# Optimization experiments

Hardware: AMD Instinct MI355X
Metric: run time of the kernel (lower is better)

## Reference

```python
import jax, jax.numpy as jnp
import numpy as np

N, E, IDIM, HLD, H, ODIM = 40000, 640000, 64, 128, 2, 1


def setup_inputs() -> dict:
    key = jax.random.key(0)
    ks = jax.random.split(key, 16)
    g = lambda i, shape, scale=0.05: (jax.random.normal(ks[i], shape, jnp.float32) * scale)
    return {
        "x": jax.random.normal(ks[0], (N, IDIM), jnp.float32),
        "edgeIdx": jax.random.randint(ks[1], (2, E), 0, N, dtype=jnp.int32),
        "edgeAttr": jax.random.normal(ks[2], (E, 4), jnp.float32),  # unused by model (passed as None)
        "enc_w0": g(3, (IDIM, HLD)), "enc_b0": jnp.zeros((HLD,), jnp.float32),
        "enc_w1": g(4, (HLD, HLD)), "enc_b1": jnp.zeros((HLD,), jnp.float32),
        "gat0_W": g(5, (HLD, H * HLD)), "gat0_bl": jnp.zeros((H * HLD,), jnp.float32),
        "gat0_att": g(6, (H, HLD)), "gat0_bias": jnp.zeros((HLD,), jnp.float32),
        "gat1_W": g(7, (HLD, H * HLD)), "gat1_bl": jnp.zeros((H * HLD,), jnp.float32),
        "gat1_att": g(8, (H, HLD)), "gat1_bias": jnp.zeros((HLD,), jnp.float32),
        "dec_w0": g(9, (HLD, HLD)), "dec_b0": jnp.zeros((HLD,), jnp.float32),
        "dec_w1": g(10, (HLD, ODIM)), "dec_b1": jnp.zeros((ODIM,), jnp.float32),
    }


def _gatv2(x, src, dst, W, bl, att, bias):
    # GATv2Conv, share_weights=True, concat=False, add_self_loops=False
    h = (x @ W + bl).reshape(N, H, HLD)                      # [N,H,C]
    e = jax.nn.leaky_relu(h[src] + h[dst], negative_slope=0.2)  # [E,H,C]
    scores = jnp.einsum('ehc,hc->eh', e, att)                # [E,H]
    m = jax.ops.segment_max(scores, dst, num_segments=N)     # per-target max
    ex = jnp.exp(scores - m[dst])
    den = jax.ops.segment_sum(ex, dst, num_segments=N)
    alpha = ex / (den[dst] + 1e-16)                          # edge softmax [E,H]
    out = jax.ops.segment_sum(alpha[:, :, None] * h[src], dst, num_segments=N)
    return out.mean(axis=1) + bias, alpha


def reference(x, edgeIdx, edgeAttr, enc_w0, enc_b0, enc_w1, enc_b1,
              gat0_W, gat0_bl, gat0_att, gat0_bias,
              gat1_W, gat1_bl, gat1_att, gat1_bias,
              dec_w0, dec_b0, dec_w1, dec_b1):
    src, dst = edgeIdx[0], edgeIdx[1]
    h = jax.nn.silu(x @ enc_w0 + enc_b0)
    h = jax.nn.silu(h @ enc_w1 + enc_b1)
    h, alpha = _gatv2(h, src, dst, gat0_W, gat0_bl, gat0_att, gat0_bias)
    h = jax.nn.silu(h)
    h, alpha = _gatv2(h, src, dst, gat1_W, gat1_bl, gat1_att, gat1_bias)
    h = jax.nn.silu(h)
    h = h @ dec_w0 + dec_b0   # decode MLP has no activations
    h = h @ dec_w1 + dec_b1
    return h, alpha.mean(axis=1)
```

## Files before the change

### kernel.cpp

```cpp
#include <hip/hip_runtime.h>
#include <hip/hip_bf16.h>
#include <math.h>

#define NN 40000
#define EE 640000
#define IDIM 64
#define HLD 128
#define NH 2
#define HH 256

typedef __attribute__((ext_vector_type(8))) short short8;
typedef __attribute__((ext_vector_type(4))) float f32x4;

__device__ __forceinline__ float silu_f(float v) {
    return v / (1.0f + expf(-v));
}
__device__ __forceinline__ unsigned short f2bf(float f) {
    unsigned u = __float_as_uint(f);
    unsigned r = (u + 0x7FFFu + ((u >> 16) & 1u)) >> 16;
    return (unsigned short)r;
}
__device__ __forceinline__ float bf2f(unsigned short b) {
    return __uint_as_float((unsigned)b << 16);
}

__global__ void k_count(const int* __restrict__ dst, int* __restrict__ counts) {
    int e = blockIdx.x * 256 + threadIdx.x;
    if (e < EE) atomicAdd(&counts[dst[e]], 1);
}

__global__ void k_blocksum(const int* __restrict__ counts, int* __restrict__ bsum) {
    __shared__ int s[256];
    int t = threadIdx.x;
    int i = blockIdx.x * 256 + t;
    s[t] = (i < NN) ? counts[i] : 0;
    __syncthreads();
    for (int o = 128; o > 0; o >>= 1) {
        if (t < o) s[t] += s[t + o];
        __syncthreads();
    }
    if (t == 0) bsum[blockIdx.x] = s[0];
}

__global__ void k_scanb(int* __restrict__ bsum, int nb) {
    __shared__ int s[256];
    int t = threadIdx.x;
    int v = (t < nb) ? bsum[t] : 0;
    s[t] = v;
    __syncthreads();
    for (int o = 1; o < 256; o <<= 1) {
        int x = 0;
        if (t >= o) x = s[t - o];
        __syncthreads();
        s[t] += x;
        __syncthreads();
    }
    if (t < nb) bsum[t] = s[t] - v;
}

__global__ void k_scatter(const int* __restrict__ counts, const int* __restrict__ bsum,
                          int* __restrict__ offsets) {
    __shared__ int s[256];
    int t = threadIdx.x;
    int i = blockIdx.x * 256 + t;
    int v = (i < NN) ? counts[i] : 0;
    s[t] = v;
    __syncthreads();
    for (int o = 1; o < 256; o <<= 1) {
        int x = 0;
        if (t >= o) x = s[t - o];
        __syncthreads();
        s[t] += x;
        __syncthreads();
    }
    if (i < NN) offsets[i] = s[t] - v + bsum[blockIdx.x];
    if (i == 0) offsets[NN] = EE;
}

__global__ void k_fill(const int* __restrict__ dst, const int* __restrict__ src,
                       const int* __restrict__ offsets,
                       int* __restrict__ cursor, int* __restrict__ ebd,
                       int* __restrict__ ebs) {
    int e = blockIdx.x * 256 + threadIdx.x;
    if (e >= EE) return;
    int d = dst[e];
    int pos = offsets[d] + atomicAdd(&cursor[d], 1);
    ebd[pos] = e;
    ebs[pos] = src[e];
}

__global__ void k_cvtX(const float* __restrict__ in, unsigned short* __restrict__ out, int n4) {
    int i = blockIdx.x * 256 + threadIdx.x;
    if (i >= n4) return;
    float4 v = *(const float4*)(in + (size_t)i * 4);
    ushort4 o;
    o.x = f2bf(v.x); o.y = f2bf(v.y); o.z = f2bf(v.z); o.w = f2bf(v.w);
    *(ushort4*)(out + (size_t)i * 4) = o;
}

__global__ void k_cvtB(const float* __restrict__ W, unsigned short* __restrict__ out,
                       int K, int N) {
    int KB = K / 32;
    int total = (N / 16) * KB * 64;
    int idx = blockIdx.x * 256 + threadIdx.x;
    if (idx >= total) return;
    int lane = idx & 63;
    int t = idx >> 6;
    int kb = t % KB, nb = t / KB;
    int n = nb * 16 + (lane & 15);
    int kbase = kb * 32 + (lane >> 4) * 8;
    unsigned short tmp[8];
    #pragma unroll
    for (int j = 0; j < 8; j++) tmp[j] = f2bf(W[(size_t)(kbase + j) * N + n]);
    uint4 o;
    o.x = (unsigned)tmp[0] | ((unsigned)tmp[1] << 16);
    o.y = (unsigned)tmp[2] | ((unsigned)tmp[3] << 16);
    o.z = (unsigned)tmp[4] | ((unsigned)tmp[5] << 16);
    o.w = (unsigned)tmp[6] | ((unsigned)tmp[7] << 16);
    *(uint4*)(out + (size_t)idx * 8) = o;
}

template <int ACT, int KB, int NB>
__global__ __launch_bounds__(256) void k_mgemm(const unsigned short* __restrict__ A,
                                               const unsigned short* __restrict__ Bp,
                                               const float* __restrict__ bias,
                                               unsigned short* __restrict__ C) {
    const int K = KB * 32, N = NB * 16;
    int tid = threadIdx.x;
    int w = tid >> 6, lane = tid & 63;
    int m0 = blockIdx.x * 64 + w * 16;
    int lr = lane & 15, lk = lane >> 4;

    f32x4 acc[NB];
    #pragma unroll
    for (int nb = 0; nb < NB; nb++) acc[nb] = f32x4{0.f, 0.f, 0.f, 0.f};

    const unsigned short* Arow = A + (size_t)(m0 + lr) * K + lk * 8;
    #pragma unroll
    for (int kb = 0; kb < KB; kb++) {
        short8 af = *(const short8*)(Arow + kb * 32);
        const unsigned short* bp = Bp + ((size_t)kb * 64 + lane) * 8;
        #pragma unroll
        for (int nb = 0; nb < NB; nb++) {
            short8 bf = *(const short8*)(bp + (size_t)nb * KB * 64 * 8);
            acc[nb] = __builtin_amdgcn_mfma_f32_16x16x32_bf16(af, bf, acc[nb], 0, 0, 0);
        }
    }

    int row0 = m0 + lk * 4;
    #pragma unroll
    for (int nb = 0; nb < NB; nb++) {
        int col = nb * 16 + lr;
        float bcol = bias[col];
        #pragma unroll
        for (int r = 0; r < 4; r++) {
            float v = acc[nb][r] + bcol;
            if (ACT) v = silu_f(v);
            C[(size_t)(row0 + r) * N + col] = f2bf(v);
        }
    }
}

template <int WRITE_SCORES>
__global__ __launch_bounds__(256) void k_fused(const unsigned short* __restrict__ hproj,
                                               const float* __restrict__ att,
                                               const int* __restrict__ offsets,
                                               const int* __restrict__ ebs,
                                               const int* __restrict__ ebd,
                                               const float* __restrict__ bias,
                                               unsigned short* __restrict__ out,
                                               float* __restrict__ scores,
                                               float2* __restrict__ statMD) {
    int t = threadIdx.x;
    int wid = t >> 6, lane = t & 63;
    int n = blockIdx.x * 4 + wid;
    int g = lane >> 4;
    int s = lane & 15;
    int h = s >> 3;
    int cb = s * 16;

    const unsigned* hp32 = (const unsigned*)hproj;

    float hd[16], at[16];
    {
        const uint4* r = (const uint4*)(hp32 + (size_t)n * 128 + s * 8);
        uint4 a0 = r[0], a1 = r[1];
        unsigned dw[8] = {a0.x, a0.y, a0.z, a0.w, a1.x, a1.y, a1.z, a1.w};
        #pragma unroll
        for (int j = 0; j < 8; j++) {
            hd[2*j]   = __uint_as_float(dw[j] << 16);
            hd[2*j+1] = __uint_as_float(dw[j] & 0xffff0000u);
        }
    }
    #pragma unroll
    for (int j = 0; j < 16; j += 4) {
        float4 a = *(const float4*)(att + cb + j);
        at[j] = a.x; at[j+1] = a.y; at[j+2] = a.z; at[j+3] = a.w;
    }

    int beg = offsets[n], end = offsets[n + 1];

    float acc[16];
    #pragma unroll
    for (int j = 0; j < 16; j++) acc[j] = 0.f;
    float den = 0.f;

    uint4 c0 = make_uint4(0,0,0,0), c1 = c0;
    if (beg + g < end) {
        const uint4* r = (const uint4*)(hp32 + (size_t)ebs[beg + g] * 128 + s * 8);
        c0 = r[0]; c1 = r[1];
    }

    for (int i = beg; i < end; i += 4) {
        bool valid = (i + g) < end;
        uint4 a0 = c0, a1 = c1;
        int ni = i + 4 + g;
        if (ni < end) {
            const uint4* r = (const uint4*)(hp32 + (size_t)ebs[ni] * 128 + s * 8);
            c0 = r[0]; c1 = r[1];
        } else {
            c0 = make_uint4(0,0,0,0); c1 = c0;
        }

        float hs[16];
        {
            unsigned dw[8] = {a0.x, a0.y, a0.z, a0.w, a1.x, a1.y, a1.z, a1.w};
            #pragma unroll
            for (int j = 0; j < 8; j++) {
                hs[2*j]   = __uint_as_float(dw[j] << 16);
                hs[2*j+1] = __uint_as_float(dw[j] & 0xffff0000u);
            }
        }
        float p0 = 0.f, p1 = 0.f;
        #pragma unroll
        for (int j = 0; j < 16; j += 2) {
            float v0 = hs[j] + hd[j];
            v0 = fmaxf(v0, 0.2f * v0);
            p0 = fmaf(v0, at[j], p0);
            float v1 = hs[j+1] + hd[j+1];
            v1 = fmaxf(v1, 0.2f * v1);
            p1 = fmaf(v1, at[j+1], p1);
        }
        float p = p0 + p1;
        p += __shfl_xor(p, 1, 64);
        p += __shfl_xor(p, 2, 64);
        p += __shfl_xor(p, 4, 64);
        p = valid ? p : -1e30f;

        if (WRITE_SCORES && valid && ((s & 7) == 0))
            scores[(size_t)ebd[i + g] * 2 + h] = p;

        float w = __expf(p);
        den += w;
        #pragma unroll
        for (int j = 0; j < 16; j++) acc[j] = fmaf(w, hs[j], acc[j]);
    }

    #pragma unroll
    for (int j = 0; j < 16; j++) {
        acc[j] += __shfl_xor(acc[j], 16, 64);
        acc[j] += __shfl_xor(acc[j], 32, 64);
    }
    den += __shfl_xor(den, 16, 64);
    den += __shfl_xor(den, 32, 64);

    if (WRITE_SCORES && (lane == 0 || lane == 8))
        statMD[(size_t)n * 2 + h] = make_float2(0.f, den);

    float inv = (den > 0.f) ? 1.0f / (den + 1e-16f) : 0.0f;
    #pragma unroll
    for (int j = 0; j < 16; j++) acc[j] *= inv;

    float om[16];
    #pragma unroll
    for (int j = 0; j < 16; j++)
        om[j] = 0.5f * (acc[j] + __shfl_xor(acc[j], 8, 64));

    if (lane < 8) {
        unsigned dwo[8];
        #pragma unroll
        for (int j = 0; j < 8; j++) {
            float v0 = silu_f(om[2*j]   + bias[cb + 2*j]);
            float v1 = silu_f(om[2*j+1] + bias[cb + 2*j + 1]);
            dwo[j] = (unsigned)f2bf(v0) | ((unsigned)f2bf(v1) << 16);
        }
        unsigned* orow = (unsigned*)(out + (size_t)n * HLD + cb);
        *(uint4*)orow       = make_uint4(dwo[0], dwo[1], dwo[2], dwo[3]);
        *(uint4*)(orow + 4) = make_uint4(dwo[4], dwo[5], dwo[6], dwo[7]);
    }
}

__global__ void k_alpha(const float* __restrict__ scores,
                        const int* __restrict__ dst,
                        const float2* __restrict__ statMD,
                        float* __restrict__ outAlpha) {
    int e = blockIdx.x * 256 + threadIdx.x;
    if (e >= EE) return;
    int d = dst[e];
    float4 md = *(const float4*)&statMD[(size_t)d * 2];
    float2 sc = *(const float2*)&scores[(size_t)e * 2];
    float a0 = __expf(sc.x) / (md.y + 1e-16f);
    float a1 = __expf(sc.y) / (md.w + 1e-16f);
    outAlpha[e] = 0.5f * (a0 + a1);
}

__global__ __launch_bounds__(256) void k_dec1(const unsigned short* __restrict__ hin,
                                              const float* __restrict__ w,
                                              const float* __restrict__ b,
                                              float* __restrict__ out) {
    int t = threadIdx.x;
    int row = blockIdx.x * 4 + (t >> 6);
    int lane = t & 63;
    if (row >= NN) return;
    const unsigned short* p = hin + (size_t)row * HLD;
    float sum = bf2f(p[lane]) * w[lane] + bf2f(p[lane + 64]) * w[lane + 64];
    #pragma unroll
    for (int o = 32; o > 0; o >>= 1) sum += __shfl_xor(sum, o, 64);
    if (lane == 0) out[row] = sum + b[0];
}

extern "C" void kernel_launch(void* const* d_in, const int* in_sizes, int n_in,
                              void* d_out, int out_size, void* d_ws, size_t ws_size,
                              hipStream_t stream) {
    const float* x       = (const float*)d_in[0];
    const int*   edgeIdx = (const int*)d_in[1];
    const float* enc_w0 = (const float*)d_in[3];
    const float* enc_b0 = (const float*)d_in[4];
    const float* enc_w1 = (const float*)d_in[5];
    const float* enc_b1 = (const float*)d_in[6];
    const float* gat_W[2]    = {(const float*)d_in[7],  (const float*)d_in[11]};
    const float* gat_bl[2]   = {(const float*)d_in[8],  (const float*)d_in[12]};
    const float* gat_att[2]  = {(const float*)d_in[9],  (const float*)d_in[13]};
    const float* gat_bias[2] = {(const float*)d_in[10], (const float*)d_in[14]};
    const float* dec_w0 = (const float*)d_in[15];
    const float* dec_b0 = (const float*)d_in[16];
    const float* dec_w1 = (const float*)d_in[17];
    const float* dec_b1 = (const float*)d_in[18];

    const int* esrc = edgeIdx;
    const int* edst = edgeIdx + EE;

    float* out = (float*)d_out;

    char* wsb = (char*)d_ws;
    float* scores  = (float*)wsb;
    float2* statMD = (float2*)(scores + (size_t)EE * 2);
    unsigned short* xbf   = (unsigned short*)(statMD + (size_t)NN * 2);
    unsigned short* hAbf  = xbf  + (size_t)NN * IDIM;
    unsigned short* hBbf  = hAbf + (size_t)NN * HLD;
    unsigned short* hproj = hBbf + (size_t)NN * HLD;
    unsigned short* wenc0p = hproj + (size_t)NN * HH;
    unsigned short* wenc1p = wenc0p + 64 * 128;
    unsigned short* wgat0p = wenc1p + 128 * 128;
    unsigned short* wgat1p = wgat0p + 128 * 256;
    unsigned short* wdec0p = wgat1p + 128 * 256;
    int* counts   = (int*)(wdec0p + 128 * 128);
    int* cursor   = counts + NN;
    int* offsets  = cursor + NN;
    int* bsum     = offsets + NN + 64;
    int* ebd      = bsum + 256;
    int* ebs      = ebd + EE;

    const int nb = (NN + 255) / 256;

    hipMemsetAsync(counts, 0, sizeof(int) * 2 * NN, stream);
    k_count<<<(EE + 255) / 256, 256, 0, stream>>>(edst, counts);
    k_blocksum<<<nb, 256, 0, stream>>>(counts, bsum);
    k_scanb<<<1, 256, 0, stream>>>(bsum, nb);
    k_scatter<<<nb, 256, 0, stream>>>(counts, bsum, offsets);
    k_fill<<<(EE + 255) / 256, 256, 0, stream>>>(edst, esrc, offsets, cursor, ebd, ebs);

    k_cvtX<<<(NN * IDIM / 4 + 255) / 256, 256, 0, stream>>>(x, xbf, NN * IDIM / 4);
    k_cvtB<<<(8 * 2 * 64 + 255) / 256, 256, 0, stream>>>(enc_w0, wenc0p, IDIM, HLD);
    k_cvtB<<<(8 * 4 * 64 + 255) / 256, 256, 0, stream>>>(enc_w1, wenc1p, HLD, HLD);
    k_cvtB<<<(16 * 4 * 64 + 255) / 256, 256, 0, stream>>>(gat_W[0], wgat0p, HLD, HH);
    k_cvtB<<<(16 * 4 * 64 + 255) / 256, 256, 0, stream>>>(gat_W[1], wgat1p, HLD, HH);
    k_cvtB<<<(8 * 4 * 64 + 255) / 256, 256, 0, stream>>>(dec_w0, wdec0p, HLD, HLD);

    k_mgemm<1, 2, 8><<<NN / 64, 256, 0, stream>>>(xbf, wenc0p, enc_b0, hAbf);
    k_mgemm<1, 4, 8><<<NN / 64, 256, 0, stream>>>(hAbf, wenc1p, enc_b1, hBbf);

    k_mgemm<0, 4, 16><<<NN / 64, 256, 0, stream>>>(hBbf, wgat0p, gat_bl[0], hproj);
    k_fused<0><<<NN / 4, 256, 0, stream>>>(hproj, gat_att[0], offsets, ebs, ebd,
                                           gat_bias[0], hAbf, nullptr, nullptr);

    k_mgemm<0, 4, 16><<<NN / 64, 256, 0, stream>>>(hAbf, wgat1p, gat_bl[1], hproj);
    k_fused<1><<<NN / 4, 256, 0, stream>>>(hproj, gat_att[1], offsets, ebs, ebd,
                                           gat_bias[1], hBbf, scores, statMD);
    k_alpha<<<(EE + 255) / 256, 256, 0, stream>>>(scores, edst, statMD, out + NN);

    k_mgemm<0, 4, 8><<<NN / 64, 256, 0, stream>>>(hBbf, wdec0p, dec_b0, hAbf);
    k_dec1<<<(NN + 3) / 4, 256, 0, stream>>>(hAbf, dec_w1, dec_b1, out);
}
```

Baseline: 450.9 us.

## Split GEMM N across waves and deepen gather prefetch in fused GAT kernel

The MFMA GEMM now uses 32-row blocks, with each pair of waves splitting the output columns in half. This doubles the grid and halves the accumulators per wave, for more occupancy and parallelism. The fused GAT aggregation loop replaces its one-ahead neighbour row prefetch with a three-deep register pipeline, plus an index prefetch one step further, to hide gather latency. The costs are more register pressure in the fused kernel and reloading the A fragments across waves in the GEMM.

Measured after the change: 442.1 us. Within noise of the previous version (-2.0%).

```diff
diff --git a/kernel.cpp b/kernel.cpp
--- a/kernel.cpp
+++ b/kernel.cpp
@@ -126,14 +126,16 @@
                                                const float* __restrict__ bias,
                                                unsigned short* __restrict__ C) {
     const int K = KB * 32, N = NB * 16;
+    const int NBH = NB / 2;
     int tid = threadIdx.x;
     int w = tid >> 6, lane = tid & 63;
-    int m0 = blockIdx.x * 64 + w * 16;
+    int m0 = blockIdx.x * 32 + (w & 1) * 16;
+    int nb0 = (w >> 1) * NBH;
     int lr = lane & 15, lk = lane >> 4;
 
-    f32x4 acc[NB];
-    #pragma unroll
-    for (int nb = 0; nb < NB; nb++) acc[nb] = f32x4{0.f, 0.f, 0.f, 0.f};
+    f32x4 acc[NBH];
+    #pragma unroll
+    for (int q = 0; q < NBH; q++) acc[q] = f32x4{0.f, 0.f, 0.f, 0.f};
 
     const unsigned short* Arow = A + (size_t)(m0 + lr) * K + lk * 8;
     #pragma unroll
@@ -141,20 +143,20 @@
         short8 af = *(const short8*)(Arow + kb * 32);
         const unsigned short* bp = Bp + ((size_t)kb * 64 + lane) * 8;
         #pragma unroll
-        for (int nb = 0; nb < NB; nb++) {
-            short8 bf = *(const short8*)(bp + (size_t)nb * KB * 64 * 8);
-            acc[nb] = __builtin_amdgcn_mfma_f32_16x16x32_bf16(af, bf, acc[nb], 0, 0, 0);
+        for (int q = 0; q < NBH; q++) {
+            short8 bf = *(const short8*)(bp + (size_t)(nb0 + q) * KB * 64 * 8);
+            acc[q] = __builtin_amdgcn_mfma_f32_16x16x32_bf16(af, bf, acc[q], 0, 0, 0);
         }
     }
 
     int row0 = m0 + lk * 4;
     #pragma unroll
-    for (int nb = 0; nb < NB; nb++) {
-        int col = nb * 16 + lr;
+    for (int q = 0; q < NBH; q++) {
+        int col = (nb0 + q) * 16 + lr;
         float bcol = bias[col];
         #pragma unroll
         for (int r = 0; r < 4; r++) {
-            float v = acc[nb][r] + bcol;
+            float v = acc[q][r] + bcol;
             if (ACT) v = silu_f(v);
             C[(size_t)(row0 + r) * N + col] = f2bf(v);
         }
@@ -205,32 +207,45 @@
     for (int j = 0; j < 16; j++) acc[j] = 0.f;
     float den = 0.f;
 
-    uint4 c0 = make_uint4(0,0,0,0), c1 = c0;
-    if (beg + g < end) {
-        const uint4* r = (const uint4*)(hp32 + (size_t)ebs[beg + g] * 128 + s * 8);
-        c0 = r[0]; c1 = r[1];
-    }
+    int j0 = beg + g;
+    int idx0 = (j0     < end) ? ebs[j0]     : 0;
+    int idx1 = (j0 + 4 < end) ? ebs[j0 + 4] : 0;
+    int idx2 = (j0 + 8 < end) ? ebs[j0 + 8] : 0;
+    uint4 b0lo, b0hi, b1lo, b1hi, b2lo, b2hi;
+    {
+        const uint4* r0 = (const uint4*)(hp32 + (size_t)idx0 * 128 + s * 8);
+        b0lo = r0[0]; b0hi = r0[1];
+        const uint4* r1 = (const uint4*)(hp32 + (size_t)idx1 * 128 + s * 8);
+        b1lo = r1[0]; b1hi = r1[1];
+        const uint4* r2 = (const uint4*)(hp32 + (size_t)idx2 * 128 + s * 8);
+        b2lo = r2[0]; b2hi = r2[1];
+    }
+    int jn = j0 + 12;
+    int idxn = (jn < end) ? ebs[jn] : 0;
+    jn += 4;
 
     for (int i = beg; i < end; i += 4) {
         bool valid = (i + g) < end;
-        uint4 a0 = c0, a1 = c1;
-        int ni = i + 4 + g;
-        if (ni < end) {
-            const uint4* r = (const uint4*)(hp32 + (size_t)ebs[ni] * 128 + s * 8);
-            c0 = r[0]; c1 = r[1];
-        } else {
-            c0 = make_uint4(0,0,0,0); c1 = c0;
-        }
 
         float hs[16];
         {
-            unsigned dw[8] = {a0.x, a0.y, a0.z, a0.w, a1.x, a1.y, a1.z, a1.w};
+            unsigned dw[8] = {b0lo.x, b0lo.y, b0lo.z, b0lo.w, b0hi.x, b0hi.y, b0hi.z, b0hi.w};
             #pragma unroll
             for (int j = 0; j < 8; j++) {
                 hs[2*j]   = __uint_as_float(dw[j] << 16);
                 hs[2*j+1] = __uint_as_float(dw[j] & 0xffff0000u);
             }
         }
+
+        b0lo = b1lo; b0hi = b1hi;
+        b1lo = b2lo; b1hi = b2hi;
+        {
+            const uint4* r = (const uint4*)(hp32 + (size_t)idxn * 128 + s * 8);
+            b2lo = r[0]; b2hi = r[1];
+        }
+        idxn = (jn < end) ? ebs[jn] : 0;
+        jn += 4;
+
         float p0 = 0.f, p1 = 0.f;
         #pragma unroll
         for (int j = 0; j < 16; j += 2) {
@@ -377,18 +392,18 @@
     k_cvtB<<<(16 * 4 * 64 + 255) / 256, 256, 0, stream>>>(gat_W[1], wgat1p, HLD, HH);
     k_cvtB<<<(8 * 4 * 64 + 255) / 256, 256, 0, stream>>>(dec_w0, wdec0p, HLD, HLD);
 
-    k_mgemm<1, 2, 8><<<NN / 64, 256, 0, stream>>>(xbf, wenc0p, enc_b0, hAbf);
-    k_mgemm<1, 4, 8><<<NN / 64, 256, 0, stream>>>(hAbf, wenc1p, enc_b1, hBbf);
-
-    k_mgemm<0, 4, 16><<<NN / 64, 256, 0, stream>>>(hBbf, wgat0p, gat_bl[0], hproj);
+    k_mgemm<1, 2, 8><<<NN / 32, 256, 0, stream>>>(xbf, wenc0p, enc_b0, hAbf);
+    k_mgemm<1, 4, 8><<<NN / 32, 256, 0, stream>>>(hAbf, wenc1p, enc_b1, hBbf);
+
+    k_mgemm<0, 4, 16><<<NN / 32, 256, 0, stream>>>(hBbf, wgat0p, gat_bl[0], hproj);
     k_fused<0><<<NN / 4, 256, 0, stream>>>(hproj, gat_att[0], offsets, ebs, ebd,
                                            gat_bias[0], hAbf, nullptr, nullptr);
 
-    k_mgemm<0, 4, 16><<<NN / 64, 256, 0, stream>>>(hAbf, wgat1p, gat_bl[1], hproj);
+    k_mgemm<0, 4, 16><<<NN / 32, 256, 0, stream>>>(hAbf, wgat1p, gat_bl[1], hproj);
     k_fused<1><<<NN / 4, 256, 0, stream>>>(hproj, gat_att[1], offsets, ebs, ebd,
                                            gat_bias[1], hBbf, scores, statMD);
     k_alpha<<<(EE + 255) / 256, 256, 0, stream>>>(scores, edst, statMD, out + NN);
 
-    k_mgemm<0, 4, 8><<<NN / 64, 256, 0, stream>>>(hBbf, wdec0p, dec_b0, hAbf);
+    k_mgemm<0, 4, 8><<<NN / 32, 256, 0, stream>>>(hBbf, wdec0p, dec_b0, hAbf);
     k_dec1<<<(NN + 3) / 4, 256, 0, stream>>>(hAbf, dec_w1, dec_b1, out);
 }
```
